# Kernel tuning notes

Measured on AMD Instinct MI355X. Metric: run time of the kernel, lower is better.

The kernel has to match this reference:

```python
import jax, jax.numpy as jnp
import numpy as np

DILATIONS = (1, 2, 4, 8, 16)
K = 3

def bn(x, g, b, m, v, eps):
    return (x - m[:, None, None]) * (g[:, None, None] / jnp.sqrt(v[:, None, None] + eps)) + b[:, None, None]

def prelu(x, a):
    return jnp.where(x > 0, x, a[:, None, None] * x)

def conv1x1(x, w):  # x: (B,C,H,W), w: (O,C)
    return jnp.einsum('bchw,oc->bohw', x, w)

def involution(x, w_red, sg, sb, sm, sv, w_span, stride, dilation, padding, w_init=None):
    # initial mapping (identity when in_channels == out_channels)
    xi = conv1x1(x, w_init) if w_init is not None else x
    B, C, H, W = xi.shape
    # unfold: patches channel layout is (C, K*K), matching torch.nn.Unfold
    patches = jax.lax.conv_general_dilated_patches(
        xi, (K, K), (stride, stride),
        padding=[(padding, padding), (padding, padding)],
        rhs_dilation=(dilation, dilation))
    Hp, Wp = patches.shape[2], patches.shape[3]
    patches = patches.reshape(B, C, K * K, Hp, Wp)
    # kernel generation from (optionally avg-pooled) original input
    if stride > 1:
        o = jax.lax.reduce_window(x, 0.0, jax.lax.add,
                                  (1, 1, stride, stride), (1, 1, stride, stride),
                                  'VALID') / float(stride * stride)
    else:
        o = x
    k = conv1x1(o, w_red)
    k = jax.nn.relu(bn(k, sg, sb, sm, sv, 1e-5))
    k = conv1x1(k, w_span)  # (B, K*K, Hp, Wp), groups=1
    # apply dynamic per-pixel kernel: broadcast over channels
    return jnp.einsum('bckhw,bkhw->bchw', patches, k)


def setup_inputs() -> dict:
    key = jax.random.key(0)
    ks = jax.random.split(key, 32)
    f32 = jnp.float32
    d = {}
    d['x'] = jax.random.normal(ks[0], (8, 32, 256, 256), f32)
    s = 0.05
    d['w1_init'] = jax.random.normal(ks[1], (64, 32), f32) * s
    d['w1_red'] = jax.random.normal(ks[2], (32, 32), f32) * s
    d['s1_g'] = jax.random.normal(ks[3], (32,), f32)
    d['s1_b'] = jax.random.normal(ks[4], (32,), f32)
    d['s1_m'] = jax.random.normal(ks[5], (32,), f32)
    d['s1_v'] = jax.random.uniform(ks[6], (32,), f32) + 0.1
    d['w1_span'] = jax.random.normal(ks[7], (9, 32), f32) * s
    d['bn1_g'] = jax.random.normal(ks[8], (64,), f32)
    d['bn1_b'] = jax.random.normal(ks[9], (64,), f32)
    d['bn1_m'] = jax.random.normal(ks[10], (64,), f32)
    d['bn1_v'] = jax.random.uniform(ks[11], (64,), f32) + 0.1
    d['pr1'] = jax.random.uniform(ks[12], (64,), f32) * 0.5
    d['wd_red'] = jax.random.normal(ks[13], (5, 64, 64), f32) * s
    d['sd_g'] = jax.random.normal(ks[14], (5, 64), f32)
    d['sd_b'] = jax.random.normal(ks[15], (5, 64), f32)
    d['sd_m'] = jax.random.normal(ks[16], (5, 64), f32)
    d['sd_v'] = jax.random.uniform(ks[17], (5, 64), f32) + 0.1
    d['wd_span'] = jax.random.normal(ks[18], (5, 9, 64), f32) * s
    d['bnd_g'] = jax.random.normal(ks[19], (5, 64), f32)
    d['bnd_b'] = jax.random.normal(ks[20], (5, 64), f32)
    d['bnd_m'] = jax.random.normal(ks[21], (5, 64), f32)
    d['bnd_v'] = jax.random.uniform(ks[22], (5, 64), f32) + 0.1
    d['prd'] = jax.random.uniform(ks[23], (5, 64), f32) * 0.5
    d['bnf_g'] = jax.random.normal(ks[24], (320,), f32)
    d['bnf_b'] = jax.random.normal(ks[25], (320,), f32)
    d['bnf_m'] = jax.random.normal(ks[26], (320,), f32)
    d['bnf_v'] = jax.random.uniform(ks[27], (320,), f32) + 0.1
    d['prf'] = jax.random.uniform(ks[28], (320,), f32) * 0.5
    return d


def reference(x, w1_init, w1_red, s1_g, s1_b, s1_m, s1_v, w1_span,
              bn1_g, bn1_b, bn1_m, bn1_v, pr1,
              wd_red, sd_g, sd_b, sd_m, sd_v, wd_span,
              bnd_g, bnd_b, bnd_m, bnd_v, prd,
              bnf_g, bnf_b, bnf_m, bnf_v, prf):
    # invo1: in=32 -> out=64, stride 2, pad 1 (uses initial 1x1 mapping)
    o1 = involution(x, w1_red, s1_g, s1_b, s1_m, s1_v, w1_span, 2, 1, 1, w_init=w1_init)
    o1 = prelu(bn(o1, bn1_g, bn1_b, bn1_m, bn1_v, 1e-3), pr1)
    outs = []
    for i, dil in enumerate(DILATIONS):
        y = involution(o1, wd_red[i], sd_g[i], sd_b[i], sd_m[i], sd_v[i],
                       wd_span[i], 1, dil, dil)
        y = prelu(bn(y, bnd_g[i], bnd_b[i], bnd_m[i], bnd_v[i], 1e-3), prd[i])
        outs.append(y)
    out = jnp.concatenate(outs, axis=1)  # (B, 320, 128, 128)
    return prelu(bn(out, bnf_g, bnf_b, bnf_m, bnf_v, 1e-3), prf)
```

## Files before the change

kernel.cpp:

```cpp
#include <hip/hip_runtime.h>

#define NPIX 16384
#define BATCH 8

__global__ void kgen1_kernel(const float* __restrict__ x,
                             const float* __restrict__ w_red,
                             const float* __restrict__ g,
                             const float* __restrict__ bta,
                             const float* __restrict__ mn,
                             const float* __restrict__ vr,
                             const float* __restrict__ w_span,
                             float* __restrict__ kout) {
    int t = blockIdx.x * blockDim.x + threadIdx.x;
    int b = t >> 14;
    int pix = t & (NPIX - 1);
    int j = pix & 127, i = pix >> 7;
    float inv[32];
    const float* xb = x + ((size_t)b * 32) * 65536 + (size_t)(2 * i) * 256 + 2 * j;
#pragma unroll
    for (int m = 0; m < 32; ++m) {
        const float2* r0 = (const float2*)(xb + (size_t)m * 65536);
        const float2* r1 = (const float2*)(xb + (size_t)m * 65536 + 256);
        float2 a = r0[0], bb = r1[0];
        inv[m] = 0.25f * ((a.x + a.y) + (bb.x + bb.y));
    }
    float kacc[9];
#pragma unroll
    for (int r = 0; r < 9; ++r) kacc[r] = 0.f;
    for (int c = 0; c < 32; ++c) {
        float a0 = 0.f, a1 = 0.f, a2 = 0.f, a3 = 0.f;
#pragma unroll
        for (int m = 0; m < 32; m += 4) {
            a0 = fmaf(w_red[c * 32 + m + 0], inv[m + 0], a0);
            a1 = fmaf(w_red[c * 32 + m + 1], inv[m + 1], a1);
            a2 = fmaf(w_red[c * 32 + m + 2], inv[m + 2], a2);
            a3 = fmaf(w_red[c * 32 + m + 3], inv[m + 3], a3);
        }
        float acc = (a0 + a1) + (a2 + a3);
        float sc = g[c] * rsqrtf(vr[c] + 1e-5f);
        float tt = (acc - mn[c]) * sc + bta[c];
        tt = tt > 0.f ? tt : 0.f;
#pragma unroll
        for (int r = 0; r < 9; ++r) kacc[r] = fmaf(w_span[r * 32 + c], tt, kacc[r]);
    }
    float* ko = kout + ((size_t)b * 9) * NPIX + pix;
#pragma unroll
    for (int r = 0; r < 9; ++r) ko[(size_t)r * NPIX] = kacc[r];
}

__global__ void applyconv_kernel(const float* __restrict__ x,
                                 const float* __restrict__ kb,
                                 const float* __restrict__ w,
                                 const float* __restrict__ g, const float* __restrict__ bt,
                                 const float* __restrict__ mn, const float* __restrict__ vr,
                                 const float* __restrict__ pr,
                                 float* __restrict__ o1) {
    __shared__ float lds_p[64][33];
    int lane = threadIdx.x & 63;
    int q = threadIdx.x >> 6;
    int gp = blockIdx.x * 64 + lane;
    int b = gp >> 14;
    int pix = gp & (NPIX - 1);
    int i = pix >> 7, j = pix & 127;
    const float* xb = x + ((size_t)b * 32) * 65536;

    float k1[9];
    const float* kp = kb + ((size_t)b * 9) * NPIX + pix;
#pragma unroll
    for (int r = 0; r < 9; ++r) k1[r] = kp[(size_t)r * NPIX];

    int y0 = 2 * i - 1;
    int coff = (j == 0) ? 0 : (2 * j - 2);
#pragma unroll
    for (int mg = 0; mg < 8; mg += 2) {
        float2 lo[2][3], hi[2][3];
#pragma unroll
        for (int mm = 0; mm < 2; ++mm) {
            const float* cb = xb + (size_t)(8 * q + mg + mm) * 65536;
#pragma unroll
            for (int ky = 0; ky < 3; ++ky) {
                int y = y0 + ky;
                int yc = y < 0 ? 0 : y;
                const float* row = cb + (size_t)yc * 256;
                lo[mm][ky] = *(const float2*)(row + coff);
                hi[mm][ky] = *(const float2*)(row + 2 * j);
            }
        }
#pragma unroll
        for (int mm = 0; mm < 2; ++mm) {
            float acc = 0.f;
#pragma unroll
            for (int ky = 0; ky < 3; ++ky) {
                int y = y0 + ky;
                float t0 = (j == 0) ? 0.f : lo[mm][ky].y;
                float t1 = hi[mm][ky].x;
                float t2 = hi[mm][ky].y;
                if (y < 0) { t0 = 0.f; t1 = 0.f; t2 = 0.f; }
                acc = fmaf(k1[3 * ky + 0], t0, acc);
                acc = fmaf(k1[3 * ky + 1], t1, acc);
                acc = fmaf(k1[3 * ky + 2], t2, acc);
            }
            lds_p[lane][8 * q + mg + mm] = acc;
        }
    }
    __syncthreads();

    float pv[32];
#pragma unroll
    for (int m = 0; m < 32; ++m) pv[m] = lds_p[lane][m];
    float* ob = o1 + ((size_t)b * 64) * NPIX + pix;
#pragma unroll
    for (int cc = 0; cc < 16; ++cc) {
        int c = 16 * q + cc;
        const float* wc = w + c * 32;
        float a0 = 0.f, a1 = 0.f, a2 = 0.f, a3 = 0.f;
#pragma unroll
        for (int m = 0; m < 32; m += 4) {
            float4 w4 = *(const float4*)(wc + m);
            a0 = fmaf(w4.x, pv[m + 0], a0);
            a1 = fmaf(w4.y, pv[m + 1], a1);
            a2 = fmaf(w4.z, pv[m + 2], a2);
            a3 = fmaf(w4.w, pv[m + 3], a3);
        }
        float sc = g[c] * rsqrtf(vr[c] + 1e-3f);
        float v = ((a0 + a1) + (a2 + a3) - mn[c]) * sc + bt[c];
        v = v > 0.f ? v : pr[c] * v;
        ob[(size_t)c * NPIX] = v;
    }
}

__global__ void kgen5_kernel(const float* __restrict__ o1,
                             const float* __restrict__ wred5,
                             const float* __restrict__ sg5, const float* __restrict__ sb5,
                             const float* __restrict__ sm5, const float* __restrict__ sv5,
                             const float* __restrict__ wspan5,
                             float* __restrict__ kout) {
    int blk = blockIdx.x;
    int q = blk >> 3;
    int s = q % 5;
    int P = (q / 5) * 8 + (blk & 7);
    int gp = P * 256 + threadIdx.x;
    int b = gp >> 14;
    int pix = gp & (NPIX - 1);
    float inv[64];
    const float* base = o1 + ((size_t)b * 64) * NPIX + pix;
#pragma unroll
    for (int m = 0; m < 64; ++m) inv[m] = base[(size_t)m * NPIX];
    const float* wr = wred5 + s * 4096;
    const float* wsp = wspan5 + s * 576;
    const float* g = sg5 + s * 64;  const float* bt = sb5 + s * 64;
    const float* mn = sm5 + s * 64; const float* vr = sv5 + s * 64;
    float kacc[9];
#pragma unroll
    for (int r = 0; r < 9; ++r) kacc[r] = 0.f;
    for (int c = 0; c < 64; ++c) {
        float a0 = 0.f, a1 = 0.f, a2 = 0.f, a3 = 0.f;
#pragma unroll
        for (int m = 0; m < 64; m += 4) {
            a0 = fmaf(wr[c * 64 + m + 0], inv[m + 0], a0);
            a1 = fmaf(wr[c * 64 + m + 1], inv[m + 1], a1);
            a2 = fmaf(wr[c * 64 + m + 2], inv[m + 2], a2);
            a3 = fmaf(wr[c * 64 + m + 3], inv[m + 3], a3);
        }
        float acc = (a0 + a1) + (a2 + a3);
        float sc = g[c] * rsqrtf(vr[c] + 1e-5f);
        float tt = (acc - mn[c]) * sc + bt[c];
        tt = tt > 0.f ? tt : 0.f;
#pragma unroll
        for (int r = 0; r < 9; ++r) kacc[r] = fmaf(wsp[r * 64 + c], tt, kacc[r]);
    }
    float* ko = kout + ((size_t)(s * BATCH + b) * 9) * NPIX + pix;
#pragma unroll
    for (int r = 0; r < 9; ++r) ko[(size_t)r * NPIX] = kacc[r];
}

template <int DIL>
__device__ __forceinline__ void invo_tap4(const float* __restrict__ xp,
                                          const float* __restrict__ kp,
                                          int i, int j0, float acc[4]) {
    constexpr int LOFF = (DIL < 4) ? 4 : DIL;
    float xw[3][12];
#pragma unroll
    for (int ky = 0; ky < 3; ++ky) {
        int y = i + DIL * (ky - 1);
        int yc = ((unsigned)y < 128u) ? y : i;
        const float* row = xp + (size_t)yc * 128;
        *(float4*)&xw[ky][0] = *(const float4*)(row + j0 - LOFF);
        *(float4*)&xw[ky][4] = *(const float4*)(row + j0);
        *(float4*)&xw[ky][8] = *(const float4*)(row + j0 + LOFF);
    }
    float kv[36];
#pragma unroll
    for (int r = 0; r < 9; ++r) *(float4*)&kv[4 * r] = *(const float4*)(kp + (size_t)r * NPIX);
#pragma unroll
    for (int ky = 0; ky < 3; ++ky) {
        int y = i + DIL * (ky - 1);
        bool yok = (unsigned)y < 128u;
#pragma unroll
        for (int kx = 0; kx < 3; ++kx) {
#pragma unroll
            for (int pp = 0; pp < 4; ++pp) {
                int xx = j0 + pp + DIL * (kx - 1);
                bool ok = yok && ((kx == 1) || ((unsigned)xx < 128u));
                int widx = 4 + pp + ((DIL < 4) ? DIL : 4) * (kx - 1);
                float xv = ok ? xw[ky][widx] : 0.f;
                acc[pp] = fmaf(xv, kv[4 * (3 * ky + kx) + pp], acc[pp]);
            }
        }
    }
}

__global__ void apply5_kernel(const float* __restrict__ o1, const float* __restrict__ kb,
                              const float* __restrict__ gd5, const float* __restrict__ bd5,
                              const float* __restrict__ md5, const float* __restrict__ vd5,
                              const float* __restrict__ ad5,
                              const float* __restrict__ gf, const float* __restrict__ bf,
                              const float* __restrict__ mf, const float* __restrict__ vf,
                              const float* __restrict__ af,
                              float* __restrict__ out) {
    int blk = blockIdx.x;
    int low3 = blk & 7;
    int c = (blk >> 3) & 63;
    int bps = (blk >> 9) * 8 + low3;
    int b = bps >> 4, ps = bps & 15;
    int pix0 = ps * 1024 + threadIdx.x * 4;
    int i = pix0 >> 7, j0 = pix0 & 127;
    const float* xp = o1 + ((size_t)(b * 64 + c)) * NPIX;

#define STAGE(S, D)                                                            \
    {                                                                          \
        float acc[4] = {0.f, 0.f, 0.f, 0.f};                                   \
        const float* kp = kb + ((size_t)(S * BATCH + b) * 9) * NPIX + pix0;    \
        invo_tap4<D>(xp, kp, i, j0, acc);                                      \
        int sc = S * 64 + c;                                                   \
        float scd = gd5[sc] * rsqrtf(vd5[sc] + 1e-3f);                         \
        float scf = gf[sc] * rsqrtf(vf[sc] + 1e-3f);                           \
        float4 o; float* op = (float*)&o;                                      \
        _Pragma("unroll")                                                      \
        for (int pp = 0; pp < 4; ++pp) {                                       \
            float v = (acc[pp] - md5[sc]) * scd + bd5[sc];                     \
            v = v > 0.f ? v : ad5[sc] * v;                                     \
            v = (v - mf[sc]) * scf + bf[sc];                                   \
            v = v > 0.f ? v : af[sc] * v;                                      \
            op[pp] = v;                                                       \
        }                                                                      \
        *(float4*)(out + ((size_t)(b * 320 + sc)) * NPIX + pix0) = o;          \
    }
    STAGE(0, 1)
    STAGE(1, 2)
    STAGE(2, 4)
    STAGE(3, 8)
    STAGE(4, 16)
#undef STAGE
}

extern "C" void kernel_launch(void* const* d_in, const int* in_sizes, int n_in,
                              void* d_out, int out_size, void* d_ws, size_t ws_size,
                              hipStream_t stream) {
    const float* x       = (const float*)d_in[0];
    const float* w1_init = (const float*)d_in[1];
    const float* w1_red  = (const float*)d_in[2];
    const float* s1_g    = (const float*)d_in[3];
    const float* s1_b    = (const float*)d_in[4];
    const float* s1_m    = (const float*)d_in[5];
    const float* s1_v    = (const float*)d_in[6];
    const float* w1_span = (const float*)d_in[7];
    const float* bn1_g   = (const float*)d_in[8];
    const float* bn1_b   = (const float*)d_in[9];
    const float* bn1_m   = (const float*)d_in[10];
    const float* bn1_v   = (const float*)d_in[11];
    const float* pr1     = (const float*)d_in[12];
    const float* wd_red  = (const float*)d_in[13];
    const float* sd_g    = (const float*)d_in[14];
    const float* sd_b    = (const float*)d_in[15];
    const float* sd_m    = (const float*)d_in[16];
    const float* sd_v    = (const float*)d_in[17];
    const float* wd_span = (const float*)d_in[18];
    const float* bnd_g   = (const float*)d_in[19];
    const float* bnd_b   = (const float*)d_in[20];
    const float* bnd_m   = (const float*)d_in[21];
    const float* bnd_v   = (const float*)d_in[22];
    const float* prd     = (const float*)d_in[23];
    const float* bnf_g   = (const float*)d_in[24];
    const float* bnf_b   = (const float*)d_in[25];
    const float* bnf_m   = (const float*)d_in[26];
    const float* bnf_v   = (const float*)d_in[27];
    const float* prf     = (const float*)d_in[28];
    float* out = (float*)d_out;

    float* ws    = (float*)d_ws;
    float* o1buf = ws + 64;
    float* k5buf = o1buf + 8388608;
    float* k1buf = k5buf + 5898240;

    const int TB = 256;

    hipLaunchKernelGGL(kgen1_kernel, dim3(BATCH * NPIX / TB), dim3(TB), 0, stream,
                       x, w1_red, s1_g, s1_b, s1_m, s1_v, w1_span, k1buf);
    hipLaunchKernelGGL(applyconv_kernel, dim3(2048), dim3(TB), 0, stream,
                       x, k1buf, w1_init, bn1_g, bn1_b, bn1_m, bn1_v, pr1, o1buf);
    hipLaunchKernelGGL(kgen5_kernel, dim3(2560), dim3(TB), 0, stream,
                       o1buf, wd_red, sd_g, sd_b, sd_m, sd_v, wd_span, k5buf);
    hipLaunchKernelGGL(apply5_kernel, dim3(8192), dim3(TB), 0, stream,
                       o1buf, k5buf,
                       bnd_g, bnd_b, bnd_m, bnd_v, prd,
                       bnf_g, bnf_b, bnf_m, bnf_v, prf,
                       out);
}
```

Before: 528.3 us.

## Fuse dilated kernel generation with involution apply into one stage kernel

```diff
diff --git a/kernel.cpp b/kernel.cpp
--- a/kernel.cpp
+++ b/kernel.cpp
@@ -2,6 +2,22 @@
 
 #define NPIX 16384
 #define BATCH 8
+
+__global__ void prep_kernel(const float* __restrict__ wred5,
+                            const float* __restrict__ sg5, const float* __restrict__ sb5,
+                            const float* __restrict__ sm5, const float* __restrict__ sv5,
+                            float* __restrict__ wrpT,
+                            float* __restrict__ bp) {
+    int t = blockIdx.x * blockDim.x + threadIdx.x;
+    if (t >= 5 * 64 * 64) return;
+    int s = t >> 12;
+    int m = (t >> 6) & 63;
+    int c = t & 63;
+    int sc_i = s * 64 + c;
+    float scd = sg5[sc_i] * rsqrtf(sv5[sc_i] + 1e-5f);
+    wrpT[(size_t)s * 4096 + m * 64 + c] = wred5[(size_t)s * 4096 + c * 64 + m] * scd;
+    if (m == 0) bp[sc_i] = sb5[sc_i] - sm5[sc_i] * scd;
+}
 
 __global__ void kgen1_kernel(const float* __restrict__ x,
                              const float* __restrict__ w_red,
@@ -129,88 +145,10 @@
     }
 }
 
-__global__ void kgen5_kernel(const float* __restrict__ o1,
-                             const float* __restrict__ wred5,
-                             const float* __restrict__ sg5, const float* __restrict__ sb5,
-                             const float* __restrict__ sm5, const float* __restrict__ sv5,
-                             const float* __restrict__ wspan5,
-                             float* __restrict__ kout) {
-    int blk = blockIdx.x;
-    int q = blk >> 3;
-    int s = q % 5;
-    int P = (q / 5) * 8 + (blk & 7);
-    int gp = P * 256 + threadIdx.x;
-    int b = gp >> 14;
-    int pix = gp & (NPIX - 1);
-    float inv[64];
-    const float* base = o1 + ((size_t)b * 64) * NPIX + pix;
-#pragma unroll
-    for (int m = 0; m < 64; ++m) inv[m] = base[(size_t)m * NPIX];
-    const float* wr = wred5 + s * 4096;
-    const float* wsp = wspan5 + s * 576;
-    const float* g = sg5 + s * 64;  const float* bt = sb5 + s * 64;
-    const float* mn = sm5 + s * 64; const float* vr = sv5 + s * 64;
-    float kacc[9];
-#pragma unroll
-    for (int r = 0; r < 9; ++r) kacc[r] = 0.f;
-    for (int c = 0; c < 64; ++c) {
-        float a0 = 0.f, a1 = 0.f, a2 = 0.f, a3 = 0.f;
-#pragma unroll
-        for (int m = 0; m < 64; m += 4) {
-            a0 = fmaf(wr[c * 64 + m + 0], inv[m + 0], a0);
-            a1 = fmaf(wr[c * 64 + m + 1], inv[m + 1], a1);
-            a2 = fmaf(wr[c * 64 + m + 2], inv[m + 2], a2);
-            a3 = fmaf(wr[c * 64 + m + 3], inv[m + 3], a3);
-        }
-        float acc = (a0 + a1) + (a2 + a3);
-        float sc = g[c] * rsqrtf(vr[c] + 1e-5f);
-        float tt = (acc - mn[c]) * sc + bt[c];
-        tt = tt > 0.f ? tt : 0.f;
-#pragma unroll
-        for (int r = 0; r < 9; ++r) kacc[r] = fmaf(wsp[r * 64 + c], tt, kacc[r]);
-    }
-    float* ko = kout + ((size_t)(s * BATCH + b) * 9) * NPIX + pix;
-#pragma unroll
-    for (int r = 0; r < 9; ++r) ko[(size_t)r * NPIX] = kacc[r];
-}
-
-template <int DIL>
-__device__ __forceinline__ void invo_tap4(const float* __restrict__ xp,
-                                          const float* __restrict__ kp,
-                                          int i, int j0, float acc[4]) {
-    constexpr int LOFF = (DIL < 4) ? 4 : DIL;
-    float xw[3][12];
-#pragma unroll
-    for (int ky = 0; ky < 3; ++ky) {
-        int y = i + DIL * (ky - 1);
-        int yc = ((unsigned)y < 128u) ? y : i;
-        const float* row = xp + (size_t)yc * 128;
-        *(float4*)&xw[ky][0] = *(const float4*)(row + j0 - LOFF);
-        *(float4*)&xw[ky][4] = *(const float4*)(row + j0);
-        *(float4*)&xw[ky][8] = *(const float4*)(row + j0 + LOFF);
-    }
-    float kv[36];
-#pragma unroll
-    for (int r = 0; r < 9; ++r) *(float4*)&kv[4 * r] = *(const float4*)(kp + (size_t)r * NPIX);
-#pragma unroll
-    for (int ky = 0; ky < 3; ++ky) {
-        int y = i + DIL * (ky - 1);
-        bool yok = (unsigned)y < 128u;
-#pragma unroll
-        for (int kx = 0; kx < 3; ++kx) {
-#pragma unroll
-            for (int pp = 0; pp < 4; ++pp) {
-                int xx = j0 + pp + DIL * (kx - 1);
-                bool ok = yok && ((kx == 1) || ((unsigned)xx < 128u));
-                int widx = 4 + pp + ((DIL < 4) ? DIL : 4) * (kx - 1);
-                float xv = ok ? xw[ky][widx] : 0.f;
-                acc[pp] = fmaf(xv, kv[4 * (3 * ky + kx) + pp], acc[pp]);
-            }
-        }
-    }
-}
-
-__global__ void apply5_kernel(const float* __restrict__ o1, const float* __restrict__ kb,
+__global__ void dstage_kernel(const float* __restrict__ o1,
+                              const float* __restrict__ wrpT,
+                              const float* __restrict__ bp,
+                              const float* __restrict__ wspan5,
                               const float* __restrict__ gd5, const float* __restrict__ bd5,
                               const float* __restrict__ md5, const float* __restrict__ vd5,
                               const float* __restrict__ ad5,
@@ -218,40 +156,111 @@
                               const float* __restrict__ mf, const float* __restrict__ vf,
                               const float* __restrict__ af,
                               float* __restrict__ out) {
+    __shared__ float pk_lds[9][4][66];
     int blk = blockIdx.x;
-    int low3 = blk & 7;
-    int c = (blk >> 3) & 63;
-    int bps = (blk >> 9) * 8 + low3;
-    int b = bps >> 4, ps = bps & 15;
-    int pix0 = ps * 1024 + threadIdx.x * 4;
-    int i = pix0 >> 7, j0 = pix0 & 127;
-    const float* xp = o1 + ((size_t)(b * 64 + c)) * NPIX;
-
-#define STAGE(S, D)                                                            \
-    {                                                                          \
-        float acc[4] = {0.f, 0.f, 0.f, 0.f};                                   \
-        const float* kp = kb + ((size_t)(S * BATCH + b) * 9) * NPIX + pix0;    \
-        invo_tap4<D>(xp, kp, i, j0, acc);                                      \
-        int sc = S * 64 + c;                                                   \
-        float scd = gd5[sc] * rsqrtf(vd5[sc] + 1e-3f);                         \
-        float scf = gf[sc] * rsqrtf(vf[sc] + 1e-3f);                           \
-        float4 o; float* op = (float*)&o;                                      \
-        _Pragma("unroll")                                                      \
-        for (int pp = 0; pp < 4; ++pp) {                                       \
-            float v = (acc[pp] - md5[sc]) * scd + bd5[sc];                     \
-            v = v > 0.f ? v : ad5[sc] * v;                                     \
-            v = (v - mf[sc]) * scf + bf[sc];                                   \
-            v = v > 0.f ? v : af[sc] * v;                                      \
-            op[pp] = v;                                                       \
-        }                                                                      \
-        *(float4*)(out + ((size_t)(b * 320 + sc)) * NPIX + pix0) = o;          \
-    }
-    STAGE(0, 1)
-    STAGE(1, 2)
-    STAGE(2, 4)
-    STAGE(3, 8)
-    STAGE(4, 16)
-#undef STAGE
+    int v = (blk & 7) * 1280 + (blk >> 3);
+    int s = v >> 11;
+    int b = (v >> 8) & 7;
+    int chunk = v & 255;
+    int i = chunk >> 1;
+    int lane = threadIdx.x & 63;
+    int q = threadIdx.x >> 6;
+    int j = ((chunk & 1) << 6) + lane;
+    int pix = i * 128 + j;
+    const float* ob = o1 + ((size_t)b * 64) * NPIX + pix;
+
+    float acc[16];
+    {
+        const float* bpc = bp + s * 64 + 16 * q;
+        float4 b0 = *(const float4*)(bpc + 0);
+        float4 b1 = *(const float4*)(bpc + 4);
+        float4 b2 = *(const float4*)(bpc + 8);
+        float4 b3 = *(const float4*)(bpc + 12);
+        acc[0] = b0.x; acc[1] = b0.y; acc[2] = b0.z; acc[3] = b0.w;
+        acc[4] = b1.x; acc[5] = b1.y; acc[6] = b1.z; acc[7] = b1.w;
+        acc[8] = b2.x; acc[9] = b2.y; acc[10] = b2.z; acc[11] = b2.w;
+        acc[12] = b3.x; acc[13] = b3.y; acc[14] = b3.z; acc[15] = b3.w;
+    }
+    const float* wT = wrpT + (size_t)s * 4096 + 16 * q;
+#pragma unroll 8
+    for (int m = 0; m < 64; ++m) {
+        float vv = ob[(size_t)m * NPIX];
+        const float* wm = wT + m * 64;
+        float4 w0 = *(const float4*)(wm + 0);
+        float4 w1 = *(const float4*)(wm + 4);
+        float4 w2 = *(const float4*)(wm + 8);
+        float4 w3 = *(const float4*)(wm + 12);
+        acc[0]  = fmaf(w0.x, vv, acc[0]);  acc[1]  = fmaf(w0.y, vv, acc[1]);
+        acc[2]  = fmaf(w0.z, vv, acc[2]);  acc[3]  = fmaf(w0.w, vv, acc[3]);
+        acc[4]  = fmaf(w1.x, vv, acc[4]);  acc[5]  = fmaf(w1.y, vv, acc[5]);
+        acc[6]  = fmaf(w1.z, vv, acc[6]);  acc[7]  = fmaf(w1.w, vv, acc[7]);
+        acc[8]  = fmaf(w2.x, vv, acc[8]);  acc[9]  = fmaf(w2.y, vv, acc[9]);
+        acc[10] = fmaf(w2.z, vv, acc[10]); acc[11] = fmaf(w2.w, vv, acc[11]);
+        acc[12] = fmaf(w3.x, vv, acc[12]); acc[13] = fmaf(w3.y, vv, acc[13]);
+        acc[14] = fmaf(w3.z, vv, acc[14]); acc[15] = fmaf(w3.w, vv, acc[15]);
+    }
+#pragma unroll
+    for (int cc = 0; cc < 16; ++cc) acc[cc] = acc[cc] > 0.f ? acc[cc] : 0.f;
+
+    const float* wsp_s = wspan5 + s * 576 + 16 * q;
+#pragma unroll
+    for (int r = 0; r < 9; ++r) {
+        const float* wr_ = wsp_s + r * 64;
+        float4 w0 = *(const float4*)(wr_ + 0);
+        float4 w1 = *(const float4*)(wr_ + 4);
+        float4 w2 = *(const float4*)(wr_ + 8);
+        float4 w3 = *(const float4*)(wr_ + 12);
+        float p0 = fmaf(w0.x, acc[0], fmaf(w0.y, acc[1], fmaf(w0.z, acc[2], w0.w * acc[3])));
+        float p1 = fmaf(w1.x, acc[4], fmaf(w1.y, acc[5], fmaf(w1.z, acc[6], w1.w * acc[7])));
+        float p2 = fmaf(w2.x, acc[8], fmaf(w2.y, acc[9], fmaf(w2.z, acc[10], w2.w * acc[11])));
+        float p3 = fmaf(w3.x, acc[12], fmaf(w3.y, acc[13], fmaf(w3.z, acc[14], w3.w * acc[15])));
+        pk_lds[r][q][lane] = (p0 + p1) + (p2 + p3);
+    }
+    __syncthreads();
+
+    float k[9];
+#pragma unroll
+    for (int r = 0; r < 9; ++r)
+        k[r] = (pk_lds[r][0][lane] + pk_lds[r][1][lane]) +
+               (pk_lds[r][2][lane] + pk_lds[r][3][lane]);
+
+    int dil = 1 << s;
+    float oacc[16];
+#pragma unroll
+    for (int cc = 0; cc < 16; ++cc) oacc[cc] = 0.f;
+    const float* cb = o1 + ((size_t)(b * 64 + 16 * q)) * NPIX;
+#pragma unroll
+    for (int ky = 0; ky < 3; ++ky) {
+        int y = i + dil * (ky - 1);
+        if ((unsigned)y >= 128u) continue;
+        const float* rowb = cb + (size_t)y * 128;
+#pragma unroll
+        for (int kx = 0; kx < 3; ++kx) {
+            int xx = j + dil * (kx - 1);
+            bool ok = (unsigned)xx < 128u;
+            int xc = ok ? xx : j;
+            float kt = k[3 * ky + kx];
+#pragma unroll
+            for (int cc = 0; cc < 16; ++cc) {
+                float vv = rowb[(size_t)cc * NPIX + xc];
+                vv = ok ? vv : 0.f;
+                oacc[cc] = fmaf(kt, vv, oacc[cc]);
+            }
+        }
+    }
+
+    float* outb = out + ((size_t)(b * 320 + s * 64 + 16 * q)) * NPIX + pix;
+#pragma unroll
+    for (int cc = 0; cc < 16; ++cc) {
+        int sc_i = s * 64 + 16 * q + cc;
+        float scd = gd5[sc_i] * rsqrtf(vd5[sc_i] + 1e-3f);
+        float scf = gf[sc_i] * rsqrtf(vf[sc_i] + 1e-3f);
+        float vv = (oacc[cc] - md5[sc_i]) * scd + bd5[sc_i];
+        vv = vv > 0.f ? vv : ad5[sc_i] * vv;
+        vv = (vv - mf[sc_i]) * scf + bf[sc_i];
+        vv = vv > 0.f ? vv : af[sc_i] * vv;
+        outb[(size_t)cc * NPIX] = vv;
+    }
 }
 
 extern "C" void kernel_launch(void* const* d_in, const int* in_sizes, int n_in,
@@ -290,19 +299,20 @@
 
     float* ws    = (float*)d_ws;
     float* o1buf = ws + 64;
-    float* k5buf = o1buf + 8388608;
-    float* k1buf = k5buf + 5898240;
+    float* k1buf = o1buf + 8388608;
+    float* wrpT  = k1buf + 1179648;
+    float* bpbuf = wrpT + 20480;
 
     const int TB = 256;
 
+    hipLaunchKernelGGL(prep_kernel, dim3(80), dim3(TB), 0, stream,
+                       wd_red, sd_g, sd_b, sd_m, sd_v, wrpT, bpbuf);
     hipLaunchKernelGGL(kgen1_kernel, dim3(BATCH * NPIX / TB), dim3(TB), 0, stream,
                        x, w1_red, s1_g, s1_b, s1_m, s1_v, w1_span, k1buf);
     hipLaunchKernelGGL(applyconv_kernel, dim3(2048), dim3(TB), 0, stream,
                        x, k1buf, w1_init, bn1_g, bn1_b, bn1_m, bn1_v, pr1, o1buf);
-    hipLaunchKernelGGL(kgen5_kernel, dim3(2560), dim3(TB), 0, stream,
-                       o1buf, wd_red, sd_g, sd_b, sd_m, sd_v, wd_span, k5buf);
-    hipLaunchKernelGGL(apply5_kernel, dim3(8192), dim3(TB), 0, stream,
-                       o1buf, k5buf,
+    hipLaunchKernelGGL(dstage_kernel, dim3(10240), dim3(TB), 0, stream,
+                       o1buf, wrpT, bpbuf, wd_span,
                        bnd_g, bnd_b, bnd_m, bnd_v, prd,
                        bnf_g, bnf_b, bnf_m, bnf_v, prf,
                        out);
```

Measured after the change: 907.3 us. 71.7% more time.
